# Kernel tuning notes

Measured on AMD Instinct MI355X. Metric: run time of the kernel, lower is better.

The kernel has to match this reference:

```python
import jax, jax.numpy as jnp
import numpy as np

BS, N, F_IN, N_HEAD, F_OUT = 8, 1024, 256, 8, 64
NEG_SLOPE = 0.2


def setup_inputs() -> dict:
    key = jax.random.key(0)
    k1, k2, k3, k4, k5 = jax.random.split(key, 5)
    h = jax.random.normal(k1, (BS, N, F_IN), dtype=jnp.float32)
    adj = jax.random.randint(k2, (BS, N, N), 0, 2, dtype=jnp.int32)
    # guarantee self-loops so every softmax row has at least one valid entry
    eye = jnp.eye(N, dtype=jnp.int32)[None]
    adj = jnp.clip(adj + eye, 0, 1)
    w = jax.random.normal(k3, (N_HEAD, F_IN, F_OUT), dtype=jnp.float32) * 0.1
    a_src = jax.random.normal(k4, (N_HEAD, F_OUT, 1), dtype=jnp.float32) * 0.1
    a_dst = jax.random.normal(k5, (N_HEAD, F_OUT, 1), dtype=jnp.float32) * 0.1
    return {"h": h, "adj": adj, "w": w, "a_src": a_src, "a_dst": a_dst}


def reference(h, adj, w, a_src, a_dst):
    # h: [b, n, f_in]; w: [h, f_in, f_out] -> h_prime: [b, h, n, f_out]
    h_prime = jnp.einsum('bnf,hfo->bhno', h, w)
    t = jnp.tanh(h_prime)
    attn_src = jnp.einsum('bhno,ho->bhn', t, a_src[..., 0])  # [b,h,n]
    attn_dst = jnp.einsum('bhno,ho->bhn', t, a_dst[..., 0])  # [b,h,n]
    # scores[b,h,i,j] = src[b,h,i] + dst[b,h,j]
    scores = attn_src[..., :, None] + attn_dst[..., None, :]
    scores = jnp.where(scores >= 0, scores, NEG_SLOPE * scores)  # leaky_relu(0.2)
    mask = (adj[:, None, :, :] > 0)  # [b,1,n,n] -> broadcast over heads
    scores = jnp.where(mask, scores, -jnp.inf)
    attn = jax.nn.softmax(scores, axis=-1)
    # dropout p=0.0 -> identity
    out = jnp.einsum('bhnm,bhmo->bhno', attn, h_prime)
    return out
```

## Files before the change

kernel.cpp:

```cpp
#include <hip/hip_runtime.h>
#include <math.h>

constexpr int CBS   = 8;
constexpr int CN    = 1024;
constexpr int CFIN  = 256;
constexpr int CNH   = 8;
constexpr int CFOUT = 64;

using f32x4 = __attribute__((ext_vector_type(4))) float;
using s16x8 = __attribute__((ext_vector_type(8))) short;

__device__ __forceinline__ short f2bf(float x) {
  __bf16 b = (__bf16)x;
  return __builtin_bit_cast(short, b);
}
__device__ __forceinline__ float bf2f(short s) {
  __bf16 b = __builtin_bit_cast(__bf16, s);
  return (float)b;
}
__device__ __forceinline__ unsigned int pkhi(float a, float b) {
  return (unsigned int)(unsigned short)f2bf(a) |
         ((unsigned int)(unsigned short)f2bf(b) << 16);
}

__global__ __launch_bounds__(256) void prep(
    const float* __restrict__ h, const float* __restrict__ w,
    const int* __restrict__ adj,
    unsigned int* __restrict__ hh, unsigned int* __restrict__ hl,
    unsigned int* __restrict__ wh, unsigned int* __restrict__ wl,
    unsigned int* __restrict__ maskT) {
  const int blk = blockIdx.x, t = threadIdx.x;
  if (blk < 1024) {
    size_t i = (size_t)blk * 256 + t;
    const int gi = (int)(i & 31);
    const int n  = (int)((i >> 5) & 1023);
    const int b  = (int)(i >> 15);
    const float4* src = (const float4*)(h + i * 8);
    float4 a = src[0], bb = src[1];
    float v[8] = {a.x, a.y, a.z, a.w, bb.x, bb.y, bb.z, bb.w};
    unsigned int hw[4], lw[4];
    #pragma unroll
    for (int p = 0; p < 4; ++p) {
      float x0 = v[2 * p], x1 = v[2 * p + 1];
      short h0 = f2bf(x0), h1 = f2bf(x1);
      hw[p] = (unsigned int)(unsigned short)h0 | ((unsigned int)(unsigned short)h1 << 16);
      lw[p] = pkhi(x0 - bf2f(h0), x1 - bf2f(h1));
    }
    const int RT = n >> 4, l15v = n & 15, kwI = gi >> 2, g4v = gi & 3;
    size_t dst = (((size_t)b * 64 + RT) * 8 + kwI) * 64 + (g4v * 16 + l15v);
    ((uint4*)hh)[dst] = make_uint4(hw[0], hw[1], hw[2], hw[3]);
    ((uint4*)hl)[dst] = make_uint4(lw[0], lw[1], lw[2], lw[3]);
  } else if (blk < 1032) {
    const int head = blk - 1024;
    const int o = t & 63, kc = (t >> 6) * 64;
    const int g = o >> 4, l15v = o & 15;
    const float* wg = w + (size_t)head * CFIN * CFOUT;
    #pragma unroll
    for (int j = 0; j < 8; ++j) {
      const int gi = (kc >> 3) + j;
      const int kwI = gi >> 2, g4v = gi & 3;
      unsigned int hw[4], lw[4];
      #pragma unroll
      for (int p = 0; p < 4; ++p) {
        int k = gi * 8 + 2 * p;
        float x0 = wg[(size_t)k * 64 + o], x1 = wg[(size_t)(k + 1) * 64 + o];
        short h0 = f2bf(x0), h1 = f2bf(x1);
        hw[p] = (unsigned int)(unsigned short)h0 | ((unsigned int)(unsigned short)h1 << 16);
        lw[p] = pkhi(x0 - bf2f(h0), x1 - bf2f(h1));
      }
      size_t dst = (((size_t)head * 4 + g) * 8 + kwI) * 64 + (g4v * 16 + l15v);
      ((uint4*)wh)[dst] = make_uint4(hw[0], hw[1], hw[2], hw[3]);
      ((uint4*)wl)[dst] = make_uint4(lw[0], lw[1], lw[2], lw[3]);
    }
  } else {
    const int lane = t & 63, wv = t >> 6;
    const long long bi = (long long)(blk - 1032) * 4 + wv;
    const int b = (int)(bi >> 10), i = (int)(bi & 1023);
    const int* ap = adj + bi * 1024 + lane;
    int a[16];
    #pragma unroll
    for (int jw = 0; jw < 16; ++jw) a[jw] = ap[jw * 64];
    #pragma unroll
    for (int jw = 0; jw < 16; ++jw) {
      unsigned long long m = __ballot(a[jw] > 0);
      if (lane == 0) {
        maskT[((size_t)b * 32 + jw * 2 + 0) * 1024 + i] = (unsigned int)m;
        maskT[((size_t)b * 32 + jw * 2 + 1) * 1024 + i] = (unsigned int)(m >> 32);
      }
    }
  }
}

__global__ __launch_bounds__(256) void liteF(
    const unsigned int* __restrict__ hh, const unsigned int* __restrict__ hl,
    const unsigned int* __restrict__ wh, const unsigned int* __restrict__ wl,
    const float* __restrict__ a_src, const float* __restrict__ a_dst,
    unsigned int* __restrict__ fBh, unsigned int* __restrict__ fBl,
    float* __restrict__ vsrc, float* __restrict__ vdst) {
  __shared__ float tileT[4][64 * 33];
  const int bid = blockIdx.x, t = threadIdx.x;
  const int lane = t & 63, wid = t >> 6;
  const int blk = (bid & 7) * 64 + (bid >> 3);
  const int bh = blk >> 3, head = bh & 7, b = bh >> 3;
  const int row0 = (blk & 7) * 128 + wid * 32;
  const int l15 = lane & 15, g4 = lane >> 4;
  const float LOG2E = 1.44269504088896340736f;

  const uint4* A0 = (const uint4*)hh + (((size_t)b * 64 + (row0 >> 4)) * 8) * 64 + lane;
  const uint4* A1 = (const uint4*)hl + (((size_t)b * 64 + (row0 >> 4)) * 8) * 64 + lane;
  const uint4* B0 = (const uint4*)wh + ((size_t)head * 4 * 8) * 64 + lane;
  const uint4* B1 = (const uint4*)wl + ((size_t)head * 4 * 8) * 64 + lane;

  f32x4 acc[2][4];
  #pragma unroll
  for (int f = 0; f < 2; ++f)
    #pragma unroll
    for (int g = 0; g < 4; ++g) acc[f][g] = (f32x4){0.f, 0.f, 0.f, 0.f};

  #pragma unroll 2
  for (int kwI = 0; kwI < 8; ++kwI) {
    s16x8 ah[2], al[2], bhf[4], blf[4];
    #pragma unroll
    for (int f = 0; f < 2; ++f) {
      ah[f] = *(const s16x8*)(A0 + (size_t)(f * 8 + kwI) * 64);
      al[f] = *(const s16x8*)(A1 + (size_t)(f * 8 + kwI) * 64);
    }
    #pragma unroll
    for (int g = 0; g < 4; ++g) {
      bhf[g] = *(const s16x8*)(B0 + (size_t)(g * 8 + kwI) * 64);
      blf[g] = *(const s16x8*)(B1 + (size_t)(g * 8 + kwI) * 64);
    }
    #pragma unroll
    for (int f = 0; f < 2; ++f)
      #pragma unroll
      for (int g = 0; g < 4; ++g) {
        acc[f][g] = __builtin_amdgcn_mfma_f32_16x16x32_bf16(ah[f], bhf[g], acc[f][g], 0, 0, 0);
        acc[f][g] = __builtin_amdgcn_mfma_f32_16x16x32_bf16(ah[f], blf[g], acc[f][g], 0, 0, 0);
        acc[f][g] = __builtin_amdgcn_mfma_f32_16x16x32_bf16(al[f], bhf[g], acc[f][g], 0, 0, 0);
      }
  }

  {
    float as4[4], ad4[4];
    #pragma unroll
    for (int g = 0; g < 4; ++g) {
      as4[g] = a_src[head * CFOUT + g * 16 + l15];
      ad4[g] = a_dst[head * CFOUT + g * 16 + l15];
    }
    #pragma unroll
    for (int f = 0; f < 2; ++f) {
      float ps[4] = {0.f, 0.f, 0.f, 0.f}, pd[4] = {0.f, 0.f, 0.f, 0.f};
      #pragma unroll
      for (int g = 0; g < 4; ++g)
        #pragma unroll
        for (int q = 0; q < 4; ++q) {
          float tv = tanhf(acc[f][g][q]);
          ps[q] += tv * as4[g];
          pd[q] += tv * ad4[g];
        }
      #pragma unroll
      for (int q = 0; q < 4; ++q) {
        #pragma unroll
        for (int mm = 1; mm < 16; mm <<= 1) {
          ps[q] += __shfl_xor(ps[q], mm, 64);
          pd[q] += __shfl_xor(pd[q], mm, 64);
        }
      }
      if (l15 == 0) {
        #pragma unroll
        for (int q = 0; q < 4; ++q) {
          int row = row0 + f * 16 + g4 * 4 + q;
          vsrc[(size_t)bh * CN + row] = ps[q] * LOG2E;
          vdst[(size_t)bh * CN + row] = pd[q] * LOG2E;
        }
      }
    }
  }

  {
    float* tw = tileT[wid];
    #pragma unroll
    for (int f = 0; f < 2; ++f)
      #pragma unroll
      for (int g = 0; g < 4; ++g)
        #pragma unroll
        for (int q = 0; q < 4; ++q)
          tw[(g * 16 + l15) * 33 + f * 16 + g4 * 4 + q] = acc[f][g][q];
    const int JT = (blk & 7) * 4 + wid;
    #pragma unroll
    for (int g = 0; g < 4; ++g) {
      float v[8];
      #pragma unroll
      for (int r = 0; r < 8; ++r)
        v[r] = tw[(g * 16 + l15) * 33 + g4 * 8 + r];
      unsigned int hw[4], lw[4];
      #pragma unroll
      for (int p = 0; p < 4; ++p) {
        float x0 = v[2 * p], x1 = v[2 * p + 1];
        short h0 = f2bf(x0), h1 = f2bf(x1);
        hw[p] = (unsigned int)(unsigned short)h0 | ((unsigned int)(unsigned short)h1 << 16);
        lw[p] = pkhi(x0 - bf2f(h0), x1 - bf2f(h1));
      }
      size_t base = (((size_t)bh * 32 + JT) * 4 + g) * 256 + (size_t)lane * 4;
      *(uint4*)(fBh + base) = make_uint4(hw[0], hw[1], hw[2], hw[3]);
      *(uint4*)(fBl + base) = make_uint4(lw[0], lw[1], lw[2], lw[3]);
    }
  }
}

__global__ __launch_bounds__(512, 4) void gat_attn_mfma(
    const unsigned int* __restrict__ maskT,
    const unsigned int* __restrict__ fBh, const unsigned int* __restrict__ fBl,
    const float* __restrict__ vsrc, const float* __restrict__ vdst,
    float* __restrict__ out) {
  __shared__ float ldsm[32 * 256 + 8 * 256];
  const int t = threadIdx.x, lane = t & 63, wid = t >> 6;
  const int w4 = wid & 3, grp = wid >> 2;
  const int bid = blockIdx.x;
  const int blk = (bid & 7) * 64 + (bid >> 3);
  const int bh = blk >> 3, b = bh >> 3;
  const int i0 = (blk & 7) * 128 + w4 * 32;
  const int l15 = lane & 15, g4 = lane >> 4;

  const float* dstp = vdst + (size_t)bh * CN;

  float M = -INFINITY;
  #pragma unroll
  for (int s_ = 0; s_ < 16; ++s_) M = fmaxf(M, dstp[s_ * 64 + lane]);
  #pragma unroll
  for (int mm = 32; mm; mm >>= 1) M = fmaxf(M, __shfl_xor(M, mm, 64));

  float sA[2], sB[2];
  #pragma unroll
  for (int f = 0; f < 2; ++f) {
    float sv = vsrc[(size_t)bh * CN + i0 + f * 16 + l15];
    float c = sv + M;
    c = fmaxf(c, 0.2f * c);
    sA[f] = sv - c;
    sB[f] = 0.2f * sv - c;
  }

  f32x4 acc[2][4], accL[2];
  #pragma unroll
  for (int f = 0; f < 2; ++f) {
    accL[f] = (f32x4){0.f, 0.f, 0.f, 0.f};
    #pragma unroll
    for (int g = 0; g < 4; ++g) acc[f][g] = (f32x4){0.f, 0.f, 0.f, 0.f};
  }

  s16x8 ones;
  {
    union { s16x8 v; unsigned int u[4]; } uo;
    unsigned int ow = (l15 == 0) ? 0x3F803F80u : 0u;
    uo.u[0] = uo.u[1] = uo.u[2] = uo.u[3] = ow;
    ones = uo.v;
  }

  const s16x8* FH = (const s16x8*)fBh + (size_t)bh * 128 * 64;
  const s16x8* FL = (const s16x8*)fBl + (size_t)bh * 128 * 64;
  const unsigned int* mT = maskT + (size_t)b * 32 * 1024;
  const int jbase = grp * 512;

  #pragma unroll 4
  for (int s = 0; s < 16; ++s) {
    const int j0 = jbase + s * 32;
    const float* dj = dstp + j0 + g4 * 8;
    float4 d0 = *(const float4*)&dj[0];
    float4 d1 = *(const float4*)&dj[4];
    float dK[8];
    dK[0] = d0.x; dK[1] = d0.y; dK[2] = d0.z; dK[3] = d0.w;
    dK[4] = d1.x; dK[5] = d1.y; dK[6] = d1.z; dK[7] = d1.w;

    const int fb0 = (j0 >> 5) * 4;
    s16x8 bhf[4], blf[4];
    #pragma unroll
    for (int g = 0; g < 4; ++g) {
      bhf[g] = FH[(size_t)(fb0 + g) * 64 + lane];
      blf[g] = FL[(size_t)(fb0 + g) * 64 + lane];
    }

    #pragma unroll
    for (int f = 0; f < 2; ++f) {
      unsigned int word = mT[(size_t)(j0 >> 5) * 1024 + i0 + f * 16 + l15];
      unsigned int byte = (word >> (g4 * 8)) & 0xFFu;
      float e[8];
      #pragma unroll
      for (int r = 0; r < 8; ++r) {
        float lr = fmaxf(sA[f] + dK[r], fmaf(0.2f, dK[r], sB[f]));
        lr = (byte & (1u << r)) ? lr : -500.f;
        e[r] = __builtin_amdgcn_exp2f(lr);
      }
      s16x8 ph;
      {
        union { s16x8 v; unsigned int u[4]; } up;
        up.u[0] = pkhi(e[0], e[1]);
        up.u[1] = pkhi(e[2], e[3]);
        up.u[2] = pkhi(e[4], e[5]);
        up.u[3] = pkhi(e[6], e[7]);
        ph = up.v;
      }
      accL[f] = __builtin_amdgcn_mfma_f32_16x16x32_bf16(ph, ones, accL[f], 0, 0, 0);
      #pragma unroll
      for (int g = 0; g < 4; ++g) {
        acc[f][g] = __builtin_amdgcn_mfma_f32_16x16x32_bf16(ph, bhf[g], acc[f][g], 0, 0, 0);
        acc[f][g] = __builtin_amdgcn_mfma_f32_16x16x32_bf16(ph, blf[g], acc[f][g], 0, 0, 0);
      }
    }
  }

  const int tid = t & 255;
  if (grp == 1) {
    #pragma unroll
    for (int f = 0; f < 2; ++f) {
      #pragma unroll
      for (int g = 0; g < 4; ++g)
        #pragma unroll
        for (int q = 0; q < 4; ++q)
          ldsm[((f * 4 + g) * 4 + q) * 256 + tid] = acc[f][g][q];
      #pragma unroll
      for (int q = 0; q < 4; ++q)
        ldsm[8192 + (f * 4 + q) * 256 + tid] = accL[f][q];
    }
  }
  __syncthreads();
  if (grp == 0) {
    #pragma unroll
    for (int f = 0; f < 2; ++f) {
      #pragma unroll
      for (int g = 0; g < 4; ++g)
        #pragma unroll
        for (int q = 0; q < 4; ++q)
          acc[f][g][q] += ldsm[((f * 4 + g) * 4 + q) * 256 + tid];
      #pragma unroll
      for (int q = 0; q < 4; ++q)
        accL[f][q] += ldsm[8192 + (f * 4 + q) * 256 + tid];
    }

    #pragma unroll
    for (int f = 0; f < 2; ++f) {
      float linv[4];
      #pragma unroll
      for (int q = 0; q < 4; ++q)
        linv[q] = 1.0f / __shfl(accL[f][q], g4 << 4, 64);
      #pragma unroll
      for (int g = 0; g < 4; ++g)
        #pragma unroll
        for (int q = 0; q < 4; ++q) {
          int row = i0 + f * 16 + g4 * 4 + q;
          int col = g * 16 + l15;
          out[((size_t)bh * CN + row) * CFOUT + col] = acc[f][g][q] * linv[q];
        }
    }
  }
}

extern "C" void kernel_launch(void* const* d_in, const int* in_sizes, int n_in,
                              void* d_out, int out_size, void* d_ws, size_t ws_size,
                              hipStream_t stream) {
  const float* h     = (const float*)d_in[0];
  const int*   adj   = (const int*)d_in[1];
  const float* w     = (const float*)d_in[2];
  const float* a_src = (const float*)d_in[3];
  const float* a_dst = (const float*)d_in[4];
  float* out = (float*)d_out;

  char* p = (char*)d_ws;
  unsigned int* hh  = (unsigned int*)p;
  unsigned int* hl  = (unsigned int*)(p + (size_t)(4u << 20));
  unsigned int* fBh = (unsigned int*)(p + (size_t)(8u << 20));
  unsigned int* fBl = (unsigned int*)(p + (size_t)(16u << 20));
  unsigned int* wh  = (unsigned int*)(p + (size_t)(24u << 20));
  unsigned int* wl  = (unsigned int*)(p + (size_t)(24u << 20) + (256u << 10));
  float* vs  = (float*)(p + (size_t)(24u << 20) + (512u << 10));
  float* vd  = (float*)(p + (size_t)(24u << 20) + (768u << 10));
  unsigned int* maskT = (unsigned int*)(p + (size_t)(25u << 20));

  hipLaunchKernelGGL(prep, dim3(1032 + 2048), dim3(256), 0, stream,
                     h, w, adj, hh, hl, wh, wl, maskT);
  hipLaunchKernelGGL(liteF, dim3(512), dim3(256), 0, stream,
                     hh, hl, wh, wl, a_src, a_dst, fBh, fBl, vs, vd);
  hipLaunchKernelGGL(gat_attn_mfma, dim3(512), dim3(512), 0, stream,
                     maskT, fBh, fBl, vs, vd, out);
}
```

Measured before the change: 76.00 us.

## Split attention kernel into 4-wave blocks with 4-way key split and tree reduction

The attention kernel now launches 2048 blocks of 256 threads. Each block owns 32 query rows and has its 4 waves each handle a quarter of the key range, 256 keys apiece. Before, 512 blocks of 512 threads had two groups of 4 waves each cover 128 rows and half the keys. Partial accumulators are combined with a two-step LDS tree reduction, so each row pays for more reduction work and more redundant loads of dst/max data. The goal is finer-grained blocks for better occupancy and load balance. The unroll pragmas on the projection k-loop and the attention loop are also removed.

```diff
diff --git a/kernel.cpp b/kernel.cpp
--- a/kernel.cpp
+++ b/kernel.cpp
@@ -117,7 +117,6 @@
     #pragma unroll
     for (int g = 0; g < 4; ++g) acc[f][g] = (f32x4){0.f, 0.f, 0.f, 0.f};
 
-  #pragma unroll 2
   for (int kwI = 0; kwI < 8; ++kwI) {
     s16x8 ah[2], al[2], bhf[4], blf[4];
     #pragma unroll
@@ -208,18 +207,17 @@
   }
 }
 
-__global__ __launch_bounds__(512, 4) void gat_attn_mfma(
+__global__ __launch_bounds__(256) void gat_attn_mfma(
     const unsigned int* __restrict__ maskT,
     const unsigned int* __restrict__ fBh, const unsigned int* __restrict__ fBl,
     const float* __restrict__ vsrc, const float* __restrict__ vdst,
     float* __restrict__ out) {
-  __shared__ float ldsm[32 * 256 + 8 * 256];
+  __shared__ float ldsm[2 * 40 * 64];
   const int t = threadIdx.x, lane = t & 63, wid = t >> 6;
-  const int w4 = wid & 3, grp = wid >> 2;
   const int bid = blockIdx.x;
-  const int blk = (bid & 7) * 64 + (bid >> 3);
-  const int bh = blk >> 3, b = bh >> 3;
-  const int i0 = (blk & 7) * 128 + w4 * 32;
+  const int blk = (bid & 7) * 256 + (bid >> 3);
+  const int bh = blk >> 5, b = bh >> 3;
+  const int i0 = (blk & 31) * 32;
   const int l15 = lane & 15, g4 = lane >> 4;
 
   const float* dstp = vdst + (size_t)bh * CN;
@@ -259,11 +257,9 @@
   const s16x8* FH = (const s16x8*)fBh + (size_t)bh * 128 * 64;
   const s16x8* FL = (const s16x8*)fBl + (size_t)bh * 128 * 64;
   const unsigned int* mT = maskT + (size_t)b * 32 * 1024;
-  const int jbase = grp * 512;
-
-  #pragma unroll 4
-  for (int s = 0; s < 16; ++s) {
-    const int j0 = jbase + s * 32;
+  const int jbase = wid * 256;
+
+  for (int j0 = jbase; j0 < jbase + 256; j0 += 32) {
     const float* dj = dstp + j0 + g4 * 8;
     float4 d0 = *(const float4*)&dj[0];
     float4 d1 = *(const float4*)&dj[4];
@@ -308,32 +304,62 @@
     }
   }
 
-  const int tid = t & 255;
-  if (grp == 1) {
+  if (wid >= 2) {
+    float* s = ldsm + (size_t)(wid - 2) * 40 * 64 + lane;
     #pragma unroll
     for (int f = 0; f < 2; ++f) {
       #pragma unroll
       for (int g = 0; g < 4; ++g)
         #pragma unroll
         for (int q = 0; q < 4; ++q)
-          ldsm[((f * 4 + g) * 4 + q) * 256 + tid] = acc[f][g][q];
+          s[((f * 4 + g) * 4 + q) * 64] = acc[f][g][q];
       #pragma unroll
       for (int q = 0; q < 4; ++q)
-        ldsm[8192 + (f * 4 + q) * 256 + tid] = accL[f][q];
+        s[(32 + f * 4 + q) * 64] = accL[f][q];
     }
   }
   __syncthreads();
-  if (grp == 0) {
+  if (wid < 2) {
+    const float* s = ldsm + (size_t)wid * 40 * 64 + lane;
     #pragma unroll
     for (int f = 0; f < 2; ++f) {
       #pragma unroll
       for (int g = 0; g < 4; ++g)
         #pragma unroll
         for (int q = 0; q < 4; ++q)
-          acc[f][g][q] += ldsm[((f * 4 + g) * 4 + q) * 256 + tid];
+          acc[f][g][q] += s[((f * 4 + g) * 4 + q) * 64];
       #pragma unroll
       for (int q = 0; q < 4; ++q)
-        accL[f][q] += ldsm[8192 + (f * 4 + q) * 256 + tid];
+        accL[f][q] += s[(32 + f * 4 + q) * 64];
+    }
+  }
+  if (wid == 1) {
+    float* s = ldsm + (size_t)40 * 64 + lane;
+    #pragma unroll
+    for (int f = 0; f < 2; ++f) {
+      #pragma unroll
+      for (int g = 0; g < 4; ++g)
+        #pragma unroll
+        for (int q = 0; q < 4; ++q)
+          s[((f * 4 + g) * 4 + q) * 64] = acc[f][g][q];
+      #pragma unroll
+      for (int q = 0; q < 4; ++q)
+        s[(32 + f * 4 + q) * 64] = accL[f][q];
+    }
+  }
+  __syncthreads();
+  if (wid == 0) {
+    const float* s = ldsm + (size_t)40 * 64 + lane;
+    #pragma unroll
+    for (int f = 0; f < 2; ++f) {
+      #pragma unroll
+      for (int g = 0; g < 4; ++g)
+        #pragma unroll
+        for (int q = 0; q < 4; ++q)
+          acc[f][g][q] += s[((f * 4 + g) * 4 + q) * 64];
+      #pragma unroll
+      for (int q = 0; q < 4; ++q)
+        accL[f][q] += s[(32 + f * 4 + q) * 64];
     }
 
     #pragma unroll
@@ -379,6 +405,6 @@
                      h, w, adj, hh, hl, wh, wl, maskT);
   hipLaunchKernelGGL(liteF, dim3(512), dim3(256), 0, stream,
                      hh, hl, wh, wl, a_src, a_dst, fBh, fBl, vs, vd);
-  hipLaunchKernelGGL(gat_attn_mfma, dim3(512), dim3(512), 0, stream,
+  hipLaunchKernelGGL(gat_attn_mfma, dim3(2048), dim3(256), 0, stream,
                      maskT, fBh, fBl, vs, vd, out);
 }
```

Measured after the change: 67.13 us. 1.13x faster.
